# Kernel optimization log

Hardware: AMD Instinct MI355X
Metric: run time of the kernel (lower is better)

The kernel has to match this reference:

```python
import jax, jax.numpy as jnp
import numpy as np

IN_F, OUT_F, R = 4096, 4096, 16
SCALING = 32.0 / R  # lora_alpha / r


def setup_inputs() -> dict:
    key = jax.random.key(0)
    kx, kw, kb, ka, kB = jax.random.split(key, 5)
    bound_w = 1.0 / np.sqrt(IN_F)  # kaiming_uniform a=sqrt(5) on (out,in) -> U(-1/sqrt(in), 1/sqrt(in))
    x = jax.random.normal(kx, (4, 4096, IN_F), dtype=jnp.float32)
    weight = jax.random.uniform(kw, (OUT_F, IN_F), jnp.float32, -bound_w, bound_w)
    bias = jax.random.uniform(kb, (OUT_F,), jnp.float32, -bound_w, bound_w)
    lora_A = jax.random.uniform(ka, (R, IN_F), jnp.float32, -bound_w, bound_w)
    # B is zero-init in the module; use small random values so the LoRA path is exercised
    lora_B = jax.random.normal(kB, (OUT_F, R), dtype=jnp.float32) * 0.01
    return {"x": x, "weight": weight, "bias": bias, "lora_A": lora_A, "lora_B": lora_B}


def reference(x, weight, bias, lora_A, lora_B):
    # base: F.linear(x, W, b) = x @ W.T + b
    base_out = jnp.einsum("bsi,oi->bso", x, weight) + bias
    # low-rank path: (x @ A.T) @ B.T * scaling  (dropout=0 -> identity)
    xr = jnp.einsum("bsi,ri->bsr", x, lora_A)  # [b, s, r]
    lora_out = jnp.einsum("bsr,or->bso", xr, lora_B) * SCALING
    return base_out + lora_out
```

## Files before the change

### kernel.cpp

```cpp
#include <hip/hip_runtime.h>
#include <hip/hip_bf16.h>


typedef __attribute__((ext_vector_type(8))) short bf16x8;
typedef __attribute__((ext_vector_type(4))) float f32x4;
typedef __attribute__((ext_vector_type(4))) unsigned short u16x4;

#define M_DIM 16384
#define N_DIM 4096
#define K_DIM 4096
#define NT 64

__device__ __forceinline__ unsigned short f2bf(float f) {
    unsigned int u = __builtin_bit_cast(unsigned int, f);
    unsigned int r = u + 0x7FFFu + ((u >> 16) & 1u);
    return (unsigned short)(r >> 16);
}

__device__ __forceinline__ void async16(const void* g, void* l) {
    __builtin_amdgcn_global_load_lds(
        (const __attribute__((address_space(1))) unsigned int*)g,
        (__attribute__((address_space(3))) unsigned int*)l,
        16, 0, 0);
}

__global__ void __launch_bounds__(256) cast_x_kernel(
    const float4* __restrict__ x, u16x4* __restrict__ y, int n4) {
    int i = blockIdx.x * blockDim.x + threadIdx.x;
    int stride = gridDim.x * blockDim.x;
    for (; i < n4; i += stride) {
        float4 v = x[i];
        u16x4 o = { f2bf(v.x), f2bf(v.y), f2bf(v.z), f2bf(v.w) };
        y[i] = o;
    }
}

__global__ void __launch_bounds__(256) weff_kernel(
    const float* __restrict__ W, const float* __restrict__ lA,
    const float* __restrict__ lB, unsigned short* __restrict__ out) {
    constexpr int K = K_DIM, R = 16;
    constexpr float S = 2.0f;
    int o = blockIdx.x;
    int t = threadIdx.x;
    float b[R];
#pragma unroll
    for (int r = 0; r < R; ++r) b[r] = lB[o * R + r];
#pragma unroll
    for (int c = 0; c < 4; ++c) {
        int i = c * 1024 + t * 4;
        float4 wv = *reinterpret_cast<const float4*>(&W[o * K + i]);
        float sx = 0.f, sy = 0.f, sz = 0.f, sw = 0.f;
#pragma unroll
        for (int r = 0; r < R; ++r) {
            float4 a = *reinterpret_cast<const float4*>(&lA[r * K + i]);
            sx += b[r] * a.x; sy += b[r] * a.y;
            sz += b[r] * a.z; sw += b[r] * a.w;
        }
        u16x4 ov = { f2bf(wv.x + S * sx), f2bf(wv.y + S * sy),
                     f2bf(wv.z + S * sz), f2bf(wv.w + S * sw) };
        *reinterpret_cast<u16x4*>(&out[o * K + i]) = ov;
    }
}

#define STAGE(G, h, tt, bsel, moff)                                           \
    do {                                                                      \
        const unsigned short* g0 = (G) +                                      \
            (size_t)((h) * 128 + wid * 16 + rc) * K_DIM + (tt) * 64 + cc * 8; \
        char* l0 = lds + (bsel) * 65536 + (moff) + (h) * 16384 + wid * 2048;  \
        async16(g0, l0);                                                      \
        async16(g0 + 8 * K_DIM, l0 + 1024);                                   \
    } while (0)

#define LDA_TO(dst, mh, bsel)                                                 \
    _Pragma("unroll") for (int mm = 0; mm < 4; ++mm)                          \
    _Pragma("unroll") for (int ks = 0; ks < 2; ++ks)                          \
        dst[mm][ks] = *(const bf16x8*)(lds + (bsel) * 65536 +                 \
            ((aBase + ((mh) * 4 + mm) * 2048) ^ (ks << 6)));

#define LDB_TO(nh, bsel)                                                      \
    _Pragma("unroll") for (int nn = 0; nn < 2; ++nn)                          \
    _Pragma("unroll") for (int ks = 0; ks < 2; ++ks)                          \
        br[(nh) * 2 + nn][ks] = *(const bf16x8*)(lds + (bsel) * 65536 +       \
            ((bBase + ((nh) * 2 + nn) * 2048) ^ (ks << 6)));

#define MM_Q(src, mh, nh)                                                     \
    __builtin_amdgcn_s_setprio(1);                                            \
    _Pragma("unroll") for (int ks = 0; ks < 2; ++ks)                          \
    _Pragma("unroll") for (int mm = 0; mm < 4; ++mm)                          \
    _Pragma("unroll") for (int nn = 0; nn < 2; ++nn)                          \
        acc[(mh) * 4 + mm][(nh) * 2 + nn] =                                   \
            __builtin_amdgcn_mfma_f32_16x16x32_bf16(                          \
                src[mm][ks], br[(nh) * 2 + nn][ks],                           \
                acc[(mh) * 4 + mm][(nh) * 2 + nn], 0, 0, 0);                  \
    __builtin_amdgcn_s_setprio(0)

#define CFENCE() asm volatile("" ::: "memory")

#define KTILE(t)                                                              \
    {                                                                         \
        const int bs_ = (t) & 1, bo_ = bs_ ^ 1;                               \
        if ((t) + 1 < NT) {                                                   \
            STAGE(Ag, 0, (t) + 1, bo_, 0);                                    \
            STAGE(Ag, 1, (t) + 1, bo_, 0);                                    \
            STAGE(Bg, 0, (t) + 1, bo_, 32768);                                \
            STAGE(Bg, 1, (t) + 1, bo_, 32768);                                \
        }                                                                     \
        LDA_TO(arA, 0, bs_);                                                  \
        LDB_TO(0, bs_);                                                       \
        LDB_TO(1, bs_);                                                       \
        MM_Q(arA, 0, 0);                                                      \
        LDA_TO(arB, 1, bs_);                                                  \
        MM_Q(arA, 0, 1);                                                      \
        MM_Q(arB, 1, 0);                                                      \
        MM_Q(arB, 1, 1);                                                      \
        asm volatile("s_waitcnt vmcnt(0)" ::: "memory");                      \
        __builtin_amdgcn_s_barrier();                                         \
        CFENCE();                                                             \
    }

__global__ void __launch_bounds__(512, 2) gemm1b_kernel(
    const unsigned short* __restrict__ A,
    const unsigned short* __restrict__ B,
    const float* __restrict__ bias,
    float* __restrict__ C) {
    __shared__ __align__(1024) char lds[131072];

    const int tid = threadIdx.x;
    const int lane = tid & 63, wid = tid >> 6;
    const int wm = wid >> 2, wn = wid & 3;
    const int lr = lane & 15, lg = lane >> 4;

    const int bid = blockIdx.x;
    const int swz = (bid & 7) * 128 + (bid >> 3);
    const int bm = swz >> 4, bn = swz & 15;

    const unsigned short* Ag = A + (size_t)bm * 256 * K_DIM;
    const unsigned short* Bg = B + (size_t)bn * 256 * K_DIM;

    const int lam = lane ^ (lane >> 3);
    const int rc = lam >> 3, cc = lam & 7;

    const int kx0 = (lg * 16) ^ ((lr & 7) << 4);
    const int aBase = (wm * 128 + lr) * 128 + kx0;
    const int bBase = 32768 + (wn * 64 + lr) * 128 + kx0;

    f32x4 acc[8][4] = {};
    bf16x8 arA[4][2], arB[4][2], br[4][2];

    STAGE(Ag, 0, 0, 0, 0);
    STAGE(Ag, 1, 0, 0, 0);
    STAGE(Bg, 0, 0, 0, 32768);
    STAGE(Bg, 1, 0, 0, 32768);
    asm volatile("s_waitcnt vmcnt(0)" ::: "memory");
    __builtin_amdgcn_s_barrier();
    CFENCE();

    for (int tt = 0; tt < NT; tt += 2) {
        KTILE(tt);
        KTILE(tt + 1);
    }

    const int row0 = bm * 256 + wm * 128;
    const int col0 = bn * 256 + wn * 64;
#pragma unroll
    for (int n = 0; n < 4; ++n) {
        const int col = col0 + n * 16 + lr;
        const float bv = bias[col];
#pragma unroll
        for (int m = 0; m < 8; ++m) {
            const int r0 = row0 + m * 16 + lg * 4;
#pragma unroll
            for (int r = 0; r < 4; ++r)
                C[(size_t)(r0 + r) * N_DIM + col] = acc[m][n][r] + bv;
        }
    }
}

extern "C" void kernel_launch(void* const* d_in, const int* in_sizes, int n_in,
                              void* d_out, int out_size, void* d_ws, size_t ws_size,
                              hipStream_t stream) {
    const float* x    = (const float*)d_in[0];
    const float* W    = (const float*)d_in[1];
    const float* bias = (const float*)d_in[2];
    const float* lA   = (const float*)d_in[3];
    const float* lB   = (const float*)d_in[4];
    float* out = (float*)d_out;

    unsigned short* xb   = (unsigned short*)d_ws;
    unsigned short* weff = (unsigned short*)((char*)d_ws + 134217728);

    cast_x_kernel<<<2048, 256, 0, stream>>>((const float4*)x, (u16x4*)xb,
                                            M_DIM * K_DIM / 4);
    weff_kernel<<<N_DIM, 256, 0, stream>>>(W, lA, lB, weff);
    gemm1b_kernel<<<(M_DIM / 256) * (N_DIM / 256), 512, 0, stream>>>(
        xb, weff, bias, out);
}
```

Before: 677.6 us.

## Restructure GEMM k-loop into two-barrier schedule prefetching B two tiles ahead

The bf16 GEMM main loop now splits each k-tile into two halves separated by a barrier. B tiles are prefetched two iterations ahead into the buffer just consumed, and A one tile ahead. A partial vmcnt(4) wait replaces the full drain, so loads stay in flight across iterations, and one A register set is reused instead of two to cut register pressure. The extra barrier per tile adds sync overhead, and the buffer-reuse timing must be exactly right to avoid races.

```diff
diff --git a/kernel.cpp b/kernel.cpp
--- a/kernel.cpp
+++ b/kernel.cpp
@@ -102,23 +102,30 @@
         if ((t) + 1 < NT) {                                                   \
             STAGE(Ag, 0, (t) + 1, bo_, 0);                                    \
             STAGE(Ag, 1, (t) + 1, bo_, 0);                                    \
-            STAGE(Bg, 0, (t) + 1, bo_, 32768);                                \
-            STAGE(Bg, 1, (t) + 1, bo_, 32768);                                \
         }                                                                     \
-        LDA_TO(arA, 0, bs_);                                                  \
+        LDA_TO(ar, 0, bs_);                                                   \
         LDB_TO(0, bs_);                                                       \
         LDB_TO(1, bs_);                                                       \
-        MM_Q(arA, 0, 0);                                                      \
-        LDA_TO(arB, 1, bs_);                                                  \
-        MM_Q(arA, 0, 1);                                                      \
-        MM_Q(arB, 1, 0);                                                      \
-        MM_Q(arB, 1, 1);                                                      \
-        asm volatile("s_waitcnt vmcnt(0)" ::: "memory");                      \
+        MM_Q(ar, 0, 0);                                                       \
+        MM_Q(ar, 0, 1);                                                       \
+        CFENCE();                                                             \
         __builtin_amdgcn_s_barrier();                                         \
         CFENCE();                                                             \
-    }
-
-__global__ void __launch_bounds__(512, 2) gemm1b_kernel(
+        if ((t) + 2 < NT) STAGE(Bg, 0, (t) + 2, bs_, 32768);                  \
+        LDA_TO(ar, 1, bs_);                                                   \
+        MM_Q(ar, 1, 0);                                                       \
+        if ((t) + 2 < NT) STAGE(Bg, 1, (t) + 2, bs_, 32768);                  \
+        MM_Q(ar, 1, 1);                                                       \
+        if ((t) < NT - 2) {                                                   \
+            asm volatile("s_waitcnt vmcnt(4)" ::: "memory");                  \
+        } else {                                                              \
+            asm volatile("s_waitcnt vmcnt(0)" ::: "memory");                  \
+        }                                                                     \
+        __builtin_amdgcn_s_barrier();                                         \
+        CFENCE();                                                             \
+    }
+
+__global__ void __launch_bounds__(512, 2) gemm2b_kernel(
     const unsigned short* __restrict__ A,
     const unsigned short* __restrict__ B,
     const float* __restrict__ bias,
@@ -145,19 +152,21 @@
     const int bBase = 32768 + (wn * 64 + lr) * 128 + kx0;
 
     f32x4 acc[8][4] = {};
-    bf16x8 arA[4][2], arB[4][2], br[4][2];
-
+    bf16x8 ar[4][2], br[4][2];
+
+    STAGE(Bg, 0, 0, 0, 32768);
+    STAGE(Bg, 1, 0, 0, 32768);
     STAGE(Ag, 0, 0, 0, 0);
     STAGE(Ag, 1, 0, 0, 0);
-    STAGE(Bg, 0, 0, 0, 32768);
-    STAGE(Bg, 1, 0, 0, 32768);
-    asm volatile("s_waitcnt vmcnt(0)" ::: "memory");
+    STAGE(Bg, 0, 1, 1, 32768);
+    STAGE(Bg, 1, 1, 1, 32768);
+    asm volatile("s_waitcnt vmcnt(4)" ::: "memory");
     __builtin_amdgcn_s_barrier();
     CFENCE();
 
-    for (int tt = 0; tt < NT; tt += 2) {
-        KTILE(tt);
-        KTILE(tt + 1);
+#pragma unroll 2
+    for (int t = 0; t < NT; ++t) {
+        KTILE(t);
     }
 
     const int row0 = bm * 256 + wm * 128;
@@ -192,6 +201,6 @@
     cast_x_kernel<<<2048, 256, 0, stream>>>((const float4*)x, (u16x4*)xb,
                                             M_DIM * K_DIM / 4);
     weff_kernel<<<N_DIM, 256, 0, stream>>>(W, lA, lB, weff);
-    gemm1b_kernel<<<(M_DIM / 256) * (N_DIM / 256), 512, 0, stream>>>(
+    gemm2b_kernel<<<(M_DIM / 256) * (N_DIM / 256), 512, 0, stream>>>(
         xb, weff, bias, out);
 }
```

Measured after the change: 593.6 us. 12.4% less time.
